# Kernel tuning notes

Measured on AMD Instinct MI355X. Metric: run time of the kernel, lower is better.

Reference implementation:

```python
import jax, jax.numpy as jnp
import numpy as np


def setup_inputs() -> dict:
    key = jax.random.key(0)
    ks = jax.random.split(key, 5)
    B, S, I, H = 64, 512, 1024, 1024
    s_ih = 1.0 / np.sqrt(I)
    s_hh = 1.0 / np.sqrt(H)
    return {
        "x": jax.random.normal(ks[0], (B, S, I), dtype=jnp.float32),
        "W_ih": jax.random.normal(ks[1], (H, I), dtype=jnp.float32) * s_ih,
        "b_ih": jax.random.normal(ks[2], (H,), dtype=jnp.float32) * s_ih,
        "W_hh": jax.random.normal(ks[3], (H, H), dtype=jnp.float32) * s_hh,
        "b_hh": jax.random.normal(ks[4], (H,), dtype=jnp.float32) * s_hh,
    }


def reference(x, W_ih, b_ih, W_hh, b_hh):
    # x: (B, S, I). Precompute the input projection for all timesteps in one GEMM.
    B, S, _ = x.shape
    H = W_hh.shape[0]
    xi = jnp.einsum("bsi,hi->bsh", x, W_ih) + b_ih  # (B, S, H)

    def step(h, xt):  # xt: (B, H)
        h_new = jnp.tanh(xt + h @ W_hh.T + b_hh)
        return h_new, h_new

    h0 = jnp.zeros((B, H), dtype=x.dtype)
    h_final, outs = jax.lax.scan(step, h0, jnp.swapaxes(xi, 0, 1))  # outs: (S, B, H)
    # Faithful to torch source: torch.cat(output, dim=0) stacks time-major
    # (S*B, H), then .view(bs, seq, H) reinterprets that buffer row-major.
    output = outs.reshape(B, S, H)
    return output, h_final
```

## Files before the change

kernel.cpp:

```cpp
#include <hip/hip_runtime.h>
#include <math.h>

#define BB 64
#define SS 512
#define II 1024
#define HH 1024

typedef _Float16 half8  __attribute__((ext_vector_type(8)));
typedef _Float16 half4_t __attribute__((ext_vector_type(4)));
typedef float    float4_t __attribute__((ext_vector_type(4)));

#define XH_OFF   0u
#define WIH_OFF  67108864u
#define WHH_OFF  69206016u
#define HBUF_OFF 71303168u
#define FLG_OFF  71565312u

__device__ __forceinline__ void load_lds16(const void* g, void* l) {
  __builtin_amdgcn_global_load_lds(
      (const __attribute__((address_space(1))) void*)g,
      (__attribute__((address_space(3))) void*)l, 16, 0, 0);
}

__global__ __launch_bounds__(256) void convert_kernel(
    const float* __restrict__ x, const float* __restrict__ Wih,
    const float* __restrict__ Whh, _Float16* __restrict__ xh,
    _Float16* __restrict__ Wihh, _Float16* __restrict__ Whhh,
    unsigned* __restrict__ flg) {
  long tid = (long)blockIdx.x * blockDim.x + threadIdx.x;
  if (tid < 1024) flg[tid] = 0;
  if (tid < 8388608L) {
    long f = tid;
    int i4 = (int)(f & 255);
    int s  = (int)((f >> 8) & 511);
    int b  = (int)(f >> 17);
    float4_t v = ((const float4_t*)x)[f];
    half4_t h;
    h[0] = (_Float16)v[0]; h[1] = (_Float16)v[1];
    h[2] = (_Float16)v[2]; h[3] = (_Float16)v[3];
    long dst = ((long)(s * 64 + b) * 1024 + i4 * 4) >> 2;
    ((half4_t*)xh)[dst] = h;
  } else if (tid < 8388608L + 262144L) {
    long f = tid - 8388608L;
    float4_t v = ((const float4_t*)Wih)[f];
    half4_t h;
    h[0] = (_Float16)v[0]; h[1] = (_Float16)v[1];
    h[2] = (_Float16)v[2]; h[3] = (_Float16)v[3];
    ((half4_t*)Wihh)[f] = h;
  } else if (tid < 8388608L + 524288L) {
    long f = tid - 8388608L - 262144L;
    float4_t v = ((const float4_t*)Whh)[f];
    half4_t h;
    h[0] = (_Float16)v[0]; h[1] = (_Float16)v[1];
    h[2] = (_Float16)v[2]; h[3] = (_Float16)v[3];
    ((half4_t*)Whhh)[f] = h;
  }
}

__global__ __launch_bounds__(256) void gemm_xi(
    const _Float16* __restrict__ Ap, const _Float16* __restrict__ Bp,
    const float* __restrict__ bias, float* __restrict__ out) {
  __shared__ _Float16 Al[128 * 32];
  __shared__ _Float16 Bl[128 * 32];
  int bid = blockIdx.x;
  int nT = bid & 7, mT = bid >> 3;
  int tid = threadIdx.x;
  int lane = tid & 63, wv = tid >> 6;
  int wm = wv & 1, wn = wv >> 1;
  int nl = lane & 15, quad = lane >> 4;
  long mBase = (long)mT * 128;
  long nBase = (long)nT * 128;
  float4_t acc[4][4] = {};

  for (int k0 = 0; k0 < 1024; k0 += 32) {
    __syncthreads();
#pragma unroll
    for (int c2 = 0; c2 < 2; ++c2) {
      int c = wv * 2 + c2;
      int flat = c * 64 + lane;
      int row = flat >> 2;
      int off = (flat & 3) * 8;
      load_lds16(Ap + (mBase + row) * 1024 + k0 + off, &Al[c * 512]);
      load_lds16(Bp + (nBase + row) * 1024 + k0 + off, &Bl[c * 512]);
    }
    __syncthreads();
    half8 af[4], bf[4];
#pragma unroll
    for (int t = 0; t < 4; ++t) {
      af[t] = *(const half8*)&Al[(wm * 64 + t * 16 + nl) * 32 + quad * 8];
      bf[t] = *(const half8*)&Bl[(wn * 64 + t * 16 + nl) * 32 + quad * 8];
    }
#pragma unroll
    for (int tm = 0; tm < 4; ++tm)
#pragma unroll
      for (int tn = 0; tn < 4; ++tn)
        acc[tm][tn] = __builtin_amdgcn_mfma_f32_16x16x32_f16(
            af[tm], bf[tn], acc[tm][tn], 0, 0, 0);
  }
#pragma unroll
  for (int tm = 0; tm < 4; ++tm) {
    long rowg = mBase + wm * 64 + tm * 16 + quad * 4;
#pragma unroll
    for (int tn = 0; tn < 4; ++tn) {
      long colg = nBase + wn * 64 + tn * 16 + nl;
      float bi = bias[colg];
#pragma unroll
      for (int r = 0; r < 4; ++r)
        out[(rowg + r) * 1024 + colg] = acc[tm][tn][r] + bi;
    }
  }
}

__global__ __launch_bounds__(256, 1) void rnn_rec(
    const _Float16* __restrict__ Whh, const float* __restrict__ bhh,
    float* __restrict__ out, _Float16* __restrict__ hbuf,
    unsigned* __restrict__ flags) {
  __shared__ _Float16 Wl[32 * 1024];
  __shared__ _Float16 hstage[64 * 32];
  const int slice = blockIdx.x;
  const int tid = threadIdx.x;
  const int wv = tid >> 6, lane = tid & 63;
  const int nl = lane & 15, quad = lane >> 4;
  const int colbase = slice * 32;

#pragma unroll 4
  for (int it = 0; it < 32; ++it) {
    int c = it * 256 + tid;
    int n = c >> 7, k8 = c & 127;
    half8 v = *(const half8*)(Whh + (long)(colbase + n) * 1024 + k8 * 8);
    *(half8*)&Wl[n * 1024 + (k8 ^ (n & 7)) * 8] = v;
  }
  __syncthreads();

  const int mycol0 = colbase + nl;
  const int mycol1 = colbase + 16 + nl;
  const float bi0 = bhh[mycol0];
  const float bi1 = bhh[mycol1];
  const int swz = (nl & 7);

#pragma unroll 1
  for (int s = 0; s < 512; ++s) {
    float xi0[4], xi1[4];
#pragma unroll
    for (int r = 0; r < 4; ++r) {
      int bat = wv * 16 + quad * 4 + r;
      xi0[r] = out[((long)s * 64 + bat) * 1024 + mycol0];
      xi1[r] = out[((long)s * 64 + bat) * 1024 + mycol1];
    }

    float4_t acc0 = {0.f, 0.f, 0.f, 0.f}, acc1 = {0.f, 0.f, 0.f, 0.f};
    if (s > 0) {
      if (wv == 0) {
        const unsigned fidx = (unsigned)(lane & 31) << 5;
        while (true) {
          unsigned f = __hip_atomic_load(&flags[fidx], __ATOMIC_RELAXED,
                                         __HIP_MEMORY_SCOPE_AGENT);
          if (__ballot(f < (unsigned)s) == 0ull) break;
          __builtin_amdgcn_s_sleep(2);
        }
      }
      __syncthreads();

      const _Float16* hp = hbuf + ((s - 1) & 1) * 65536 +
                           ((wv * 16 + nl) << 10) + quad * 8;
      float4_t hf[32];
      __builtin_amdgcn_sched_barrier(0);
#pragma unroll
      for (int kt = 0; kt < 32; ++kt)
        asm volatile("global_load_dwordx4 %0, %1, off sc0 sc1"
                     : "=v"(hf[kt]) : "v"(hp + kt * 32));
      asm volatile("s_waitcnt vmcnt(0)" ::: "memory");
      __builtin_amdgcn_sched_barrier(0);
#pragma unroll
      for (int kt = 0; kt < 32; ++kt) {
        half8 a = __builtin_bit_cast(half8, hf[kt]);
        half8 b0 = *(const half8*)&Wl[nl * 1024 + ((kt * 4 + quad) ^ swz) * 8];
        half8 b1 = *(const half8*)&Wl[(16 + nl) * 1024 +
                                      ((kt * 4 + quad) ^ swz) * 8];
        acc0 = __builtin_amdgcn_mfma_f32_16x16x32_f16(a, b0, acc0, 0, 0, 0);
        acc1 = __builtin_amdgcn_mfma_f32_16x16x32_f16(a, b1, acc1, 0, 0, 0);
      }
    }

    float hv0[4], hv1[4];
#pragma unroll
    for (int r = 0; r < 4; ++r) {
      int bat = wv * 16 + quad * 4 + r;
      float pre0 = acc0[r] + xi0[r] + bi0;
      float e0 = __expf(2.f * pre0);
      float v0 = 1.f - 2.f / (e0 + 1.f);
      hv0[r] = v0;
      hstage[bat * 32 + nl] = (_Float16)v0;
      float pre1 = acc1[r] + xi1[r] + bi1;
      float e1 = __expf(2.f * pre1);
      float v1 = 1.f - 2.f / (e1 + 1.f);
      hv1[r] = v1;
      hstage[bat * 32 + 16 + nl] = (_Float16)v1;
    }
    __syncthreads();

    {
      int bat = tid >> 2, ch = tid & 3;
      float4_t pv = *(const float4_t*)&hstage[bat * 32 + ch * 8];
      _Float16* dst = hbuf + (s & 1) * 65536 + bat * 1024 + colbase + ch * 8;
      asm volatile("global_store_dwordx4 %0, %1, off sc0 sc1"
                   :: "v"(dst), "v"(pv) : "memory");
    }
    __syncthreads();
    if (tid == 0)
      __hip_atomic_store(&flags[(unsigned)slice << 5], (unsigned)(s + 1),
                         __ATOMIC_RELAXED, __HIP_MEMORY_SCOPE_AGENT);

#pragma unroll
    for (int r = 0; r < 4; ++r) {
      int bat = wv * 16 + quad * 4 + r;
      out[((long)s * 64 + bat) * 1024 + mycol0] = hv0[r];
      out[((long)s * 64 + bat) * 1024 + mycol1] = hv1[r];
      if (s == 511) {
        out[33554432L + bat * 1024 + mycol0] = hv0[r];
        out[33554432L + bat * 1024 + mycol1] = hv1[r];
      }
    }
  }
}

extern "C" void kernel_launch(void* const* d_in, const int* in_sizes, int n_in,
                              void* d_out, int out_size, void* d_ws,
                              size_t ws_size, hipStream_t stream) {
  const float* x   = (const float*)d_in[0];
  const float* Wih = (const float*)d_in[1];
  const float* bih = (const float*)d_in[2];
  const float* Whh = (const float*)d_in[3];
  const float* bhh = (const float*)d_in[4];
  char* ws = (char*)d_ws;
  _Float16* xh   = (_Float16*)(ws + XH_OFF);
  _Float16* Wihh = (_Float16*)(ws + WIH_OFF);
  _Float16* Whhh = (_Float16*)(ws + WHH_OFF);
  _Float16* hbuf = (_Float16*)(ws + HBUF_OFF);
  unsigned* flg  = (unsigned*)(ws + FLG_OFF);
  float* out = (float*)d_out;

  convert_kernel<<<34816, 256, 0, stream>>>(x, Wih, Whh, xh, Wihh, Whhh, flg);
  gemm_xi<<<2048, 256, 0, stream>>>(xh, Wihh, bih, out);
  rnn_rec<<<32, 256, 0, stream>>>(Whhh, bhh, out, hbuf, flg);
}
```

Measured before the change: 3.387 ms.

## Split recurrent GEMM over K across waves with register-resident W_hh and per-wave flags

The recurrent kernel now has each wave own a quarter of the K dimension and keep its W_hh fragments in registers instead of LDS. Each wave loads h for all 64 batch rows over its K range, and partial sums are reduced through a double-buffered LDS array. Synchronisation moves from one flag per block to one per wave, and each wave spins on its own flags, which removes two block barriers per step. The aim is to cut LDS traffic and per-step latency, at the cost of a cross-wave reduction and more flag polling.

```diff
diff --git a/kernel.cpp b/kernel.cpp
--- a/kernel.cpp
+++ b/kernel.cpp
@@ -115,110 +115,127 @@
     const _Float16* __restrict__ Whh, const float* __restrict__ bhh,
     float* __restrict__ out, _Float16* __restrict__ hbuf,
     unsigned* __restrict__ flags) {
-  __shared__ _Float16 Wl[32 * 1024];
-  __shared__ _Float16 hstage[64 * 32];
+  __shared__ __align__(16) float red[2][4][4][2][256];
+  __shared__ __align__(16) _Float16 hstage[4][512];
   const int slice = blockIdx.x;
   const int tid = threadIdx.x;
   const int wv = tid >> 6, lane = tid & 63;
   const int nl = lane & 15, quad = lane >> 4;
   const int colbase = slice * 32;
 
-#pragma unroll 4
-  for (int it = 0; it < 32; ++it) {
-    int c = it * 256 + tid;
-    int n = c >> 7, k8 = c & 127;
-    half8 v = *(const half8*)(Whh + (long)(colbase + n) * 1024 + k8 * 8);
-    *(half8*)&Wl[n * 1024 + (k8 ^ (n & 7)) * 8] = v;
-  }
-  __syncthreads();
-
-  const int mycol0 = colbase + nl;
-  const int mycol1 = colbase + 16 + nl;
-  const float bi0 = bhh[mycol0];
-  const float bi1 = bhh[mycol1];
-  const int swz = (nl & 7);
+  half8 wfrag[2][8];
+#pragma unroll
+  for (int n = 0; n < 2; ++n)
+#pragma unroll
+    for (int t = 0; t < 8; ++t)
+      wfrag[n][t] = *(const half8*)(Whh + (long)(colbase + n * 16 + nl) * 1024 +
+                                    wv * 256 + t * 32 + quad * 8);
+
+  const int mycol0 = colbase + nl, mycol1 = colbase + 16 + nl;
+  const float bi0 = bhh[mycol0], bi1 = bhh[mycol1];
+  const int mybat = wv * 16 + quad * 4;
+  const int ri = nl * 16 + quad * 4;
 
 #pragma unroll 1
   for (int s = 0; s < 512; ++s) {
     float xi0[4], xi1[4];
 #pragma unroll
     for (int r = 0; r < 4; ++r) {
-      int bat = wv * 16 + quad * 4 + r;
-      xi0[r] = out[((long)s * 64 + bat) * 1024 + mycol0];
-      xi1[r] = out[((long)s * 64 + bat) * 1024 + mycol1];
-    }
-
-    float4_t acc0 = {0.f, 0.f, 0.f, 0.f}, acc1 = {0.f, 0.f, 0.f, 0.f};
+      long rowo = ((long)s * 64 + mybat + r) * 1024;
+      xi0[r] = out[rowo + mycol0];
+      xi1[r] = out[rowo + mycol1];
+    }
+
+    float4_t acc[4][2] = {};
     if (s > 0) {
-      if (wv == 0) {
-        const unsigned fidx = (unsigned)(lane & 31) << 5;
+      {
+        const unsigned widx = ((unsigned)(wv * 32 + (lane & 31))) << 3;
         while (true) {
-          unsigned f = __hip_atomic_load(&flags[fidx], __ATOMIC_RELAXED,
+          unsigned f = __hip_atomic_load(&flags[widx], __ATOMIC_RELAXED,
                                          __HIP_MEMORY_SCOPE_AGENT);
           if (__ballot(f < (unsigned)s) == 0ull) break;
-          __builtin_amdgcn_s_sleep(2);
+          __builtin_amdgcn_s_sleep(1);
         }
       }
-      __syncthreads();
-
-      const _Float16* hp = hbuf + ((s - 1) & 1) * 65536 +
-                           ((wv * 16 + nl) << 10) + quad * 8;
-      float4_t hf[32];
+      const _Float16* hb = hbuf + ((s - 1) & 1) * 65536 + wv * 256 + quad * 8;
+      float4_t hf[4][8];
       __builtin_amdgcn_sched_barrier(0);
 #pragma unroll
-      for (int kt = 0; kt < 32; ++kt)
-        asm volatile("global_load_dwordx4 %0, %1, off sc0 sc1"
-                     : "=v"(hf[kt]) : "v"(hp + kt * 32));
+      for (int m = 0; m < 4; ++m)
+#pragma unroll
+        for (int t = 0; t < 8; ++t)
+          asm volatile("global_load_dwordx4 %0, %1, off sc0 sc1"
+                       : "=v"(hf[m][t])
+                       : "v"(hb + ((m * 16 + nl) << 10) + t * 32));
       asm volatile("s_waitcnt vmcnt(0)" ::: "memory");
       __builtin_amdgcn_sched_barrier(0);
 #pragma unroll
-      for (int kt = 0; kt < 32; ++kt) {
-        half8 a = __builtin_bit_cast(half8, hf[kt]);
-        half8 b0 = *(const half8*)&Wl[nl * 1024 + ((kt * 4 + quad) ^ swz) * 8];
-        half8 b1 = *(const half8*)&Wl[(16 + nl) * 1024 +
-                                      ((kt * 4 + quad) ^ swz) * 8];
-        acc0 = __builtin_amdgcn_mfma_f32_16x16x32_f16(a, b0, acc0, 0, 0, 0);
-        acc1 = __builtin_amdgcn_mfma_f32_16x16x32_f16(a, b1, acc1, 0, 0, 0);
-      }
+      for (int t = 0; t < 8; ++t)
+#pragma unroll
+        for (int m = 0; m < 4; ++m) {
+          half8 a = __builtin_bit_cast(half8, hf[m][t]);
+          acc[m][0] = __builtin_amdgcn_mfma_f32_16x16x32_f16(
+              a, wfrag[0][t], acc[m][0], 0, 0, 0);
+          acc[m][1] = __builtin_amdgcn_mfma_f32_16x16x32_f16(
+              a, wfrag[1][t], acc[m][1], 0, 0, 0);
+        }
+    }
+
+#pragma unroll
+    for (int m = 0; m < 4; ++m)
+#pragma unroll
+      for (int n = 0; n < 2; ++n)
+        *(float4_t*)&red[s & 1][wv][m][n][ri] = acc[m][n];
+    __syncthreads();
+    float4_t fin0, fin1;
+    {
+      float4_t a0 = *(const float4_t*)&red[s & 1][0][wv][0][ri];
+      float4_t b0 = *(const float4_t*)&red[s & 1][1][wv][0][ri];
+      float4_t c0 = *(const float4_t*)&red[s & 1][2][wv][0][ri];
+      float4_t d0 = *(const float4_t*)&red[s & 1][3][wv][0][ri];
+      fin0 = (a0 + b0) + (c0 + d0);
+      float4_t a1 = *(const float4_t*)&red[s & 1][0][wv][1][ri];
+      float4_t b1 = *(const float4_t*)&red[s & 1][1][wv][1][ri];
+      float4_t c1 = *(const float4_t*)&red[s & 1][2][wv][1][ri];
+      float4_t d1 = *(const float4_t*)&red[s & 1][3][wv][1][ri];
+      fin1 = (a1 + b1) + (c1 + d1);
     }
 
     float hv0[4], hv1[4];
 #pragma unroll
     for (int r = 0; r < 4; ++r) {
-      int bat = wv * 16 + quad * 4 + r;
-      float pre0 = acc0[r] + xi0[r] + bi0;
+      float pre0 = fin0[r] + xi0[r] + bi0;
       float e0 = __expf(2.f * pre0);
       float v0 = 1.f - 2.f / (e0 + 1.f);
       hv0[r] = v0;
-      hstage[bat * 32 + nl] = (_Float16)v0;
-      float pre1 = acc1[r] + xi1[r] + bi1;
+      hstage[wv][(quad * 4 + r) * 32 + nl] = (_Float16)v0;
+      float pre1 = fin1[r] + xi1[r] + bi1;
       float e1 = __expf(2.f * pre1);
       float v1 = 1.f - 2.f / (e1 + 1.f);
       hv1[r] = v1;
-      hstage[bat * 32 + 16 + nl] = (_Float16)v1;
-    }
-    __syncthreads();
-
+      hstage[wv][(quad * 4 + r) * 32 + 16 + nl] = (_Float16)v1;
+    }
     {
-      int bat = tid >> 2, ch = tid & 3;
-      float4_t pv = *(const float4_t*)&hstage[bat * 32 + ch * 8];
-      _Float16* dst = hbuf + (s & 1) * 65536 + bat * 1024 + colbase + ch * 8;
+      float4_t pv = *(const float4_t*)&hstage[wv][(lane >> 2) * 32 + (lane & 3) * 8];
+      _Float16* dst = hbuf + (s & 1) * 65536 +
+                      ((wv * 16 + (lane >> 2)) << 10) + colbase + (lane & 3) * 8;
       asm volatile("global_store_dwordx4 %0, %1, off sc0 sc1"
                    :: "v"(dst), "v"(pv) : "memory");
-    }
-    __syncthreads();
-    if (tid == 0)
-      __hip_atomic_store(&flags[(unsigned)slice << 5], (unsigned)(s + 1),
-                         __ATOMIC_RELAXED, __HIP_MEMORY_SCOPE_AGENT);
+      asm volatile("s_waitcnt vmcnt(0)" ::: "memory");
+      if (lane == 0)
+        __hip_atomic_store(&flags[((unsigned)(slice * 4 + wv)) << 3],
+                           (unsigned)(s + 1), __ATOMIC_RELAXED,
+                           __HIP_MEMORY_SCOPE_AGENT);
+    }
 
 #pragma unroll
     for (int r = 0; r < 4; ++r) {
-      int bat = wv * 16 + quad * 4 + r;
-      out[((long)s * 64 + bat) * 1024 + mycol0] = hv0[r];
-      out[((long)s * 64 + bat) * 1024 + mycol1] = hv1[r];
+      long rowo = ((long)s * 64 + mybat + r) * 1024;
+      out[rowo + mycol0] = hv0[r];
+      out[rowo + mycol1] = hv1[r];
       if (s == 511) {
-        out[33554432L + bat * 1024 + mycol0] = hv0[r];
-        out[33554432L + bat * 1024 + mycol1] = hv1[r];
+        out[33554432L + (mybat + r) * 1024 + mycol0] = hv0[r];
+        out[33554432L + (mybat + r) * 1024 + mycol1] = hv1[r];
       }
     }
   }
```

Result: no change. 3.423 ms (+1.1%).
